# Kernel tuning notes

Hardware: AMD Instinct MI355X
Metric: run time of the kernel (lower is better)

## Reference

```python
import jax, jax.numpy as jnp
import numpy as np

N = 100000   # nodes
E = 1600000  # edges (avg degree 16)
D = 128      # in = hidden = out channels
DROP_P = 0.2


def setup_inputs() -> dict:
    key = jax.random.key(0)
    ks = jax.random.split(key, 11)
    s = 1.0 / np.sqrt(D)  # glorot-ish scale
    inp = {
        "features": jax.random.normal(ks[0], (N, D), jnp.float32),
        "edge_index": jax.random.randint(ks[1], (2, E), 0, N, dtype=jnp.int64),
    }
    for i in range(3):
        inp[f"Wl{i}"] = jax.random.normal(ks[2 + 3 * i], (D, D), jnp.float32) * s
        inp[f"Wr{i}"] = jax.random.normal(ks[3 + 3 * i], (D, D), jnp.float32) * s
        inp[f"b{i}"] = jnp.zeros((D,), jnp.float32)
    return inp


def _sage_conv(x, src, dst, Wl, Wr, b):
    # PyG SAGEConv (aggr='max'): out = lin_l(max_{j->i} x_j) + lin_r(x_i)
    agg = jax.ops.segment_max(x[src], dst, num_segments=N)  # [N, D_in]
    agg = jnp.where(jnp.isfinite(agg), agg, 0.0)  # isolated nodes -> 0 (torch_scatter zero-init)
    return agg @ Wl + x @ Wr + b


def _dropout(x, key, p=DROP_P):
    keep = jax.random.bernoulli(key, 1.0 - p, x.shape)
    return jnp.where(keep, x / (1.0 - p), 0.0)


def reference(features, edge_index, Wl0, Wr0, b0, Wl1, Wr1, b1, Wl2, Wr2, b2):
    src, dst = edge_index[0], edge_index[1]
    k1, k2 = jax.random.split(jax.random.key(42))
    x = _sage_conv(features, src, dst, Wl0, Wr0, b0)
    x = _dropout(jax.nn.elu(x), k1)
    x = _sage_conv(x, src, dst, Wl1, Wr1, b1)
    x = _dropout(jax.nn.elu(x), k2)
    x = _sage_conv(x, src, dst, Wl2, Wr2, b2)
    return x
```

## Files before the change

### kernel.cpp

```cpp
#include <hip/hip_runtime.h>
#include <math.h>

#define D 128
#define BSHIFT 9
#define BCAP 12288

typedef __attribute__((ext_vector_type(8))) _Float16 half8;
typedef __attribute__((ext_vector_type(4))) float floatx4;

__host__ __device__ __forceinline__ unsigned rotl32(unsigned v, int r) {
  return (v << r) | (v >> (32 - r));
}

__host__ __device__ __forceinline__ void threefry2x32(unsigned k0, unsigned k1,
                                                      unsigned x0, unsigned x1,
                                                      unsigned &o0, unsigned &o1) {
  unsigned ks2 = k0 ^ k1 ^ 0x1BD11BDAu;
  unsigned v0 = x0 + k0;
  unsigned v1 = x1 + k1;
  v0 += v1; v1 = rotl32(v1, 13); v1 ^= v0;
  v0 += v1; v1 = rotl32(v1, 15); v1 ^= v0;
  v0 += v1; v1 = rotl32(v1, 26); v1 ^= v0;
  v0 += v1; v1 = rotl32(v1, 6);  v1 ^= v0;
  v0 += k1; v1 += ks2 + 1u;
  v0 += v1; v1 = rotl32(v1, 17); v1 ^= v0;
  v0 += v1; v1 = rotl32(v1, 29); v1 ^= v0;
  v0 += v1; v1 = rotl32(v1, 16); v1 ^= v0;
  v0 += v1; v1 = rotl32(v1, 24); v1 ^= v0;
  v0 += ks2; v1 += k0 + 2u;
  v0 += v1; v1 = rotl32(v1, 13); v1 ^= v0;
  v0 += v1; v1 = rotl32(v1, 15); v1 ^= v0;
  v0 += v1; v1 = rotl32(v1, 26); v1 ^= v0;
  v0 += v1; v1 = rotl32(v1, 6);  v1 ^= v0;
  v0 += k0; v1 += k1 + 3u;
  v0 += v1; v1 = rotl32(v1, 17); v1 ^= v0;
  v0 += v1; v1 = rotl32(v1, 29); v1 ^= v0;
  v0 += v1; v1 = rotl32(v1, 16); v1 ^= v0;
  v0 += v1; v1 = rotl32(v1, 24); v1 ^= v0;
  v0 += k1; v1 += ks2 + 4u;
  v0 += v1; v1 = rotl32(v1, 13); v1 ^= v0;
  v0 += v1; v1 = rotl32(v1, 15); v1 ^= v0;
  v0 += v1; v1 = rotl32(v1, 26); v1 ^= v0;
  v0 += v1; v1 = rotl32(v1, 6);  v1 ^= v0;
  v0 += ks2; v1 += k0 + 5u;
  o0 = v0; o1 = v1;
}

__device__ __forceinline__ unsigned short f2h(float f) {
  _Float16 h = (_Float16)f;
  return *(unsigned short*)&h;
}

__device__ __forceinline__ unsigned pkmax(unsigned a, unsigned b) {
  unsigned r;
  asm("v_pk_max_f16 %0, %1, %2" : "=v"(r) : "v"(a), "v"(b));
  return r;
}


__global__ __launch_bounds__(256) void bucket_count_kernel(
    const int* __restrict__ dst, int* __restrict__ bucketTotal, int nEdges) {
  __shared__ int lc[256];
  int t = threadIdx.x;
  lc[t] = 0;
  __syncthreads();
  int e0 = blockIdx.x * 4096;
  for (int i = t; i < 4096; i += 256) {
    int e = e0 + i;
    if (e < nEdges) atomicAdd(&lc[dst[e] >> BSHIFT], 1);
  }
  __syncthreads();
  int c = lc[t];
  if (c > 0) atomicAdd(&bucketTotal[t], c);
}

__global__ __launch_bounds__(256) void scan_buckets_kernel(
    const int* __restrict__ bucketTotal, int* __restrict__ buckOff,
    int* __restrict__ bucketCursor, int nBuck) {
  __shared__ int s[256];
  int t = threadIdx.x;
  int v = (t < nBuck) ? bucketTotal[t] : 0;
  s[t] = v;
  __syncthreads();
  for (int off = 1; off < 256; off <<= 1) {
    int u = (t >= off) ? s[t - off] : 0;
    __syncthreads();
    s[t] += u;
    __syncthreads();
  }
  int excl = s[t] - v;
  if (t < nBuck) {
    buckOff[t] = excl;
    bucketCursor[t] = excl;
  } else if (t == nBuck) {
    buckOff[t] = s[255];
  }
}

__global__ __launch_bounds__(256) void bucket_scatter_kernel(
    const int* __restrict__ src, const int* __restrict__ dst,
    int* __restrict__ bucketCursor, unsigned* __restrict__ pairs,
    int nEdges, int nBuck) {
  __shared__ int lcount[256];
  __shared__ int lbase[256];
  __shared__ int loff[256];
  int t = threadIdx.x;
  lcount[t] = 0; loff[t] = 0;
  __syncthreads();
  int e0 = blockIdx.x * 4096;
  for (int i = t; i < 4096; i += 256) {
    int e = e0 + i;
    if (e < nEdges) atomicAdd(&lcount[dst[e] >> BSHIFT], 1);
  }
  __syncthreads();
  if (t < nBuck) {
    int c = lcount[t];
    if (c > 0) lbase[t] = atomicAdd(&bucketCursor[t], c);
  }
  __syncthreads();
  for (int i = t; i < 4096; i += 256) {
    int e = e0 + i;
    if (e < nEdges) {
      int d = dst[e];
      int b = d >> BSHIFT;
      int lp = atomicAdd(&loff[b], 1);
      pairs[lbase[b] + lp] = ((unsigned)src[e] << BSHIFT) | ((unsigned)d & 511u);
    }
  }
}

__global__ __launch_bounds__(256) void local_fill_kernel(
    const unsigned* __restrict__ pairs, const int* __restrict__ buckOff,
    int* __restrict__ rowStart, int* __restrict__ csrSrc,
    int nNodes, int nBuck) {
  __shared__ int sData[BCAP];
  __shared__ int lcnt[1 << BSHIFT];
  __shared__ int sSum[256];
  int b = blockIdx.x;
  int node0 = b << BSHIFT;
  int base = buckOff[b];
  int end = buckOff[b + 1];
  int cnt = end - base;
  int t = threadIdx.x;

  lcnt[t] = 0;
  lcnt[t + 256] = 0;
  __syncthreads();

  for (int i = base + t; i < end; i += 256)
    atomicAdd(&lcnt[pairs[i] & 511u], 1);
  __syncthreads();

  int c0 = lcnt[2 * t];
  int c1 = lcnt[2 * t + 1];
  int local = c0 + c1;
  sSum[t] = local;
  __syncthreads();
  for (int off = 1; off < 256; off <<= 1) {
    int v = (t >= off) ? sSum[t - off] : 0;
    __syncthreads();
    sSum[t] += v;
    __syncthreads();
  }
  int excl = sSum[t] - local;
  __syncthreads();
  lcnt[2 * t] = excl;
  lcnt[2 * t + 1] = excl + c0;
  int n0 = node0 + 2 * t;
  int n1 = n0 + 1;
  if (n0 < nNodes) rowStart[n0] = base + excl;
  if (n1 < nNodes) rowStart[n1] = base + excl + c0;
  if (b == nBuck - 1 && t == 255) rowStart[nNodes] = end;
  __syncthreads();

  if (cnt <= BCAP) {
    for (int i = base + t; i < end; i += 256) {
      unsigned p = pairs[i];
      int lp = atomicAdd(&lcnt[p & 511u], 1);
      sData[lp] = (int)(p >> BSHIFT);
    }
    __syncthreads();
    for (int i = t; i < cnt; i += 256)
      csrSrc[base + i] = sData[i];
  } else {
    for (int i = base + t; i < end; i += 256) {
      unsigned p = pairs[i];
      int lp = atomicAdd(&lcnt[p & 511u], 1);
      csrSrc[base + lp] = (int)(p >> BSHIFT);
    }
  }
}

__global__ __launch_bounds__(256) void convert_feat_kernel(
    const float* __restrict__ f, unsigned short* __restrict__ o, int nElems) {
  int i = (blockIdx.x * 256 + threadIdx.x) * 4;
  if (i + 3 < nElems) {
    float4 v = *((const float4*)(f + i));
    unsigned a = (unsigned)f2h(v.x) | ((unsigned)f2h(v.y) << 16);
    unsigned b = (unsigned)f2h(v.z) | ((unsigned)f2h(v.w) << 16);
    *((uint2*)(o + i)) = make_uint2(a, b);
  } else {
    for (int j = i; j < nElems; ++j) o[j] = f2h(f[j]);
  }
}

__global__ __launch_bounds__(256) void pack_weights_kernel(
    const float* __restrict__ Wl0, const float* __restrict__ Wr0,
    const float* __restrict__ Wl1, const float* __restrict__ Wr1,
    const float* __restrict__ Wl2, const float* __restrict__ Wr2,
    unsigned short* __restrict__ Wt) {
  int t = blockIdx.x * 256 + threadIdx.x;
  if (t >= 3 * 128 * 256) return;
  int l = t >> 15;
  int rem = t & 32767;
  int n = rem >> 8;
  int k = rem & 255;
  const float* Wl = (l == 0) ? Wl0 : (l == 1) ? Wl1 : Wl2;
  const float* Wr = (l == 0) ? Wr0 : (l == 1) ? Wr1 : Wr2;
  float v = (k < 128) ? Wl[k * D + n] : Wr[(k - 128) * D + n];
  Wt[t] = f2h(v);
}

__global__ __launch_bounds__(256) void gather_max_f16_kernel(
    const uint4* __restrict__ x8, const int* __restrict__ rowStart,
    const int* __restrict__ csrSrc, uint4* __restrict__ agg8, int nNodes) {
  int n = blockIdx.x * 4 + (threadIdx.x >> 6);
  if (n >= nNodes) return;
  int lane = threadIdx.x & 63;
  int q = lane >> 4;
  int l16 = lane & 15;
  int e0 = rowStart[n], e1 = rowStart[n + 1];
  unsigned m0 = 0xFC00FC00u, m1 = 0xFC00FC00u,
           m2 = 0xFC00FC00u, m3 = 0xFC00FC00u;
  int e = e0;
  for (; e + 7 < e1; e += 8) {
    int sa = csrSrc[e + q];
    int sb = csrSrc[e + 4 + q];
    uint4 va = x8[(size_t)sa * 16 + l16];
    uint4 vb = x8[(size_t)sb * 16 + l16];
    m0 = pkmax(m0, pkmax(va.x, vb.x));
    m1 = pkmax(m1, pkmax(va.y, vb.y));
    m2 = pkmax(m2, pkmax(va.z, vb.z));
    m3 = pkmax(m3, pkmax(va.w, vb.w));
  }
  if (e + 3 < e1) {
    int sa = csrSrc[e + q];
    uint4 va = x8[(size_t)sa * 16 + l16];
    m0 = pkmax(m0, va.x); m1 = pkmax(m1, va.y);
    m2 = pkmax(m2, va.z); m3 = pkmax(m3, va.w);
    e += 4;
  }
  for (; e < e1; ++e) {
    int sa = csrSrc[e];
    uint4 va = x8[(size_t)sa * 16 + l16];
    m0 = pkmax(m0, va.x); m1 = pkmax(m1, va.y);
    m2 = pkmax(m2, va.z); m3 = pkmax(m3, va.w);
  }
  m0 = pkmax(m0, (unsigned)__shfl_xor((int)m0, 16, 64));
  m1 = pkmax(m1, (unsigned)__shfl_xor((int)m1, 16, 64));
  m2 = pkmax(m2, (unsigned)__shfl_xor((int)m2, 16, 64));
  m3 = pkmax(m3, (unsigned)__shfl_xor((int)m3, 16, 64));
  m0 = pkmax(m0, (unsigned)__shfl_xor((int)m0, 32, 64));
  m1 = pkmax(m1, (unsigned)__shfl_xor((int)m1, 32, 64));
  m2 = pkmax(m2, (unsigned)__shfl_xor((int)m2, 32, 64));
  m3 = pkmax(m3, (unsigned)__shfl_xor((int)m3, 32, 64));
  uint4 r = make_uint4(0u, 0u, 0u, 0u);
  if (e0 != e1) r = make_uint4(m0, m1, m2, m3);
  if (q == 0) agg8[(size_t)n * 16 + l16] = r;
}

#define PA 280

__global__ __launch_bounds__(256) void fused_mfma_kernel(
    const unsigned short* __restrict__ agghf, unsigned short* __restrict__ xhf,
    const unsigned short* __restrict__ Wt, const float* __restrict__ bias,
    float* __restrict__ outF, int nRows, int mode, unsigned kk0, unsigned kk1) {
  __shared__ unsigned short sA[32 * PA];

  const int tid = threadIdx.x;
  const int row0 = blockIdx.x * 32;
  const int wv = tid >> 6, lane = tid & 63;
  const int quad = lane >> 4, m16 = lane & 15;
  const int nbase = wv * 32;

#pragma unroll
  for (int i = 0; i < 4; ++i) {
    int idx = i * 256 + tid;
    int r = idx >> 5;
    int seg = idx & 31;
    uint4 v = make_uint4(0, 0, 0, 0);
    if (row0 + r < nRows) {
      if (seg < 16) v = ((const uint4*)(agghf + (size_t)(row0 + r) * D))[seg];
      else          v = ((const uint4*)(xhf  + (size_t)(row0 + r) * D))[seg - 16];
    }
    *((uint4*)(sA + r * PA + seg * 8)) = v;
  }

  half8 bfr[2][4][2];
#pragma unroll
  for (int kc = 0; kc < 2; ++kc)
#pragma unroll
    for (int ks = 0; ks < 4; ++ks)
#pragma unroll
      for (int j = 0; j < 2; ++j)
        bfr[kc][ks][j] = *((const half8*)(
            Wt + (size_t)(nbase + j * 16 + m16) * 256 + kc * 128 + ks * 32 + quad * 8));

  floatx4 acc[2][2];
#pragma unroll
  for (int i = 0; i < 2; ++i)
#pragma unroll
    for (int j = 0; j < 2; ++j) acc[i][j] = (floatx4)(0.0f);

  __syncthreads();

#pragma unroll
  for (int kc = 0; kc < 2; ++kc)
#pragma unroll
    for (int ks = 0; ks < 4; ++ks) {
      int kA = kc * 128 + ks * 32 + quad * 8;
      half8 a0 = *((const half8*)(sA + m16 * PA + kA));
      half8 a1 = *((const half8*)(sA + (m16 + 16) * PA + kA));
      acc[0][0] = __builtin_amdgcn_mfma_f32_16x16x32_f16(a0, bfr[kc][ks][0], acc[0][0], 0, 0, 0);
      acc[0][1] = __builtin_amdgcn_mfma_f32_16x16x32_f16(a0, bfr[kc][ks][1], acc[0][1], 0, 0, 0);
      acc[1][0] = __builtin_amdgcn_mfma_f32_16x16x32_f16(a1, bfr[kc][ks][0], acc[1][0], 0, 0, 0);
      acc[1][1] = __builtin_amdgcn_mfma_f32_16x16x32_f16(a1, bfr[kc][ks][1], acc[1][1], 0, 0, 0);
    }

#pragma unroll
  for (int j = 0; j < 2; ++j) {
    int col = nbase + j * 16 + m16;
    float bc = bias[col];
#pragma unroll
    for (int i = 0; i < 2; ++i) {
#pragma unroll
      for (int reg = 0; reg < 4; ++reg) {
        int r = row0 + i * 16 + quad * 4 + reg;
        if (r >= nRows) continue;
        float v = acc[i][j][reg] + bc;
        if (mode < 2) {
          v = (v > 0.0f) ? v : expm1f(v);
          unsigned jj = (unsigned)r * D + col;
          unsigned y0, y1;
          threefry2x32(kk0, kk1, 0u, jj, y0, y1);
          float u = __uint_as_float((((y0 ^ y1) >> 9)) | 0x3F800000u) - 1.0f;
          v = (u < 0.8f) ? v * 1.25f : 0.0f;
          xhf[(size_t)r * D + col] = f2h(v);
        } else {
          outF[(size_t)r * D + col] = v;
        }
      }
    }
  }
}

extern "C" void kernel_launch(void* const* d_in, const int* in_sizes, int n_in,
                              void* d_out, int out_size, void* d_ws, size_t ws_size,
                              hipStream_t stream) {
  const float* feat = (const float*)d_in[0];
  const int* ei = (const int*)d_in[1];
  const float* Wl0 = (const float*)d_in[2];
  const float* Wr0 = (const float*)d_in[3];
  const float* b0 = (const float*)d_in[4];
  const float* Wl1 = (const float*)d_in[5];
  const float* Wr1 = (const float*)d_in[6];
  const float* b1 = (const float*)d_in[7];
  const float* Wl2 = (const float*)d_in[8];
  const float* Wr2 = (const float*)d_in[9];
  const float* b2 = (const float*)d_in[10];

  const int N = in_sizes[0] / D;
  const int E = in_sizes[1] / 2;
  const int* src = ei;
  const int* dst = ei + E;

  const size_t hfBytes = (size_t)N * D * 2;
  char* wsp = (char*)d_ws;
  size_t off = 0;
  unsigned short* xhf   = (unsigned short*)(wsp + off); off += hfBytes;
  unsigned short* agghf = (unsigned short*)(wsp + off); off += hfBytes;
  unsigned short* Wt    = (unsigned short*)(wsp + off); off += ((size_t)3 * 128 * 256 * 2 + 511) & ~511ull;
  int* rowStart     = (int*)(wsp + off); off += ((size_t)(N + 1) * 4 + 511) & ~511ull;
  int* bucketTotal  = (int*)(wsp + off); off += 2048;
  int* buckOff      = (int*)(wsp + off); off += 2048;
  int* bucketCursor = (int*)(wsp + off); off += 2048;
  int* csrSrc    = (int*)(wsp + off); off += (size_t)E * 4;
  unsigned* pairs = (unsigned*)(wsp + off); off += (size_t)E * 4;

  const int nBuck = (N + (1 << BSHIFT) - 1) >> BSHIFT;

  unsigned k1a, k1b, k2a, k2b;
  threefry2x32(0u, 42u, 0u, 0u, k1a, k1b);
  threefry2x32(0u, 42u, 0u, 1u, k2a, k2b);

  hipMemsetAsync(bucketTotal, 0, 1024, stream);
  bucket_count_kernel<<<(E + 4095) / 4096, 256, 0, stream>>>(dst, bucketTotal, E);
  scan_buckets_kernel<<<1, 256, 0, stream>>>(bucketTotal, buckOff, bucketCursor, nBuck);
  bucket_scatter_kernel<<<(E + 4095) / 4096, 256, 0, stream>>>(src, dst, bucketCursor, pairs, E, nBuck);
  local_fill_kernel<<<nBuck, 256, 0, stream>>>(pairs, buckOff, rowStart, csrSrc, N, nBuck);

  convert_feat_kernel<<<(N * D / 4 + 255) / 256, 256, 0, stream>>>(feat, xhf, N * D);
  pack_weights_kernel<<<(3 * 128 * 256 + 255) / 256, 256, 0, stream>>>(
      Wl0, Wr0, Wl1, Wr1, Wl2, Wr2, Wt);

  dim3 blk(256);
  dim3 grdMax((N + 3) / 4);
  dim3 grdGemm((N + 31) / 32);
  float* outF = (float*)d_out;

  gather_max_f16_kernel<<<grdMax, blk, 0, stream>>>((const uint4*)xhf, rowStart, csrSrc, (uint4*)agghf, N);
  fused_mfma_kernel<<<grdGemm, blk, 0, stream>>>(agghf, xhf, Wt, b0, outF, N, 0, k1a, k1b);

  gather_max_f16_kernel<<<grdMax, blk, 0, stream>>>((const uint4*)xhf, rowStart, csrSrc, (uint4*)agghf, N);
  fused_mfma_kernel<<<grdGemm, blk, 0, stream>>>(agghf, xhf, Wt + 32768, b1, outF, N, 1, k2a, k2b);

  gather_max_f16_kernel<<<grdMax, blk, 0, stream>>>((const uint4*)xhf, rowStart, csrSrc, (uint4*)agghf, N);
  fused_mfma_kernel<<<grdGemm, blk, 0, stream>>>(agghf, xhf, Wt + 65536, b2, outF, N, 2, 0u, 0u);
}
```

Measured before the change: 521.9 us.

## Fuse neighbor max-gather into the MFMA layer kernel with ping-pong buffers

Merges the separate gather-max kernel into the GEMM kernel: each block gathers max-aggregated neighbor rows for its 32 nodes straight into shared memory, then runs the MFMA and epilogue. Two feature buffers are ping-ponged so a layer never overwrites inputs other blocks still read. This removes the agg buffer write and read round trip and three launches per run. The gather now runs with 8 rows per wave serially inside a larger block, which may cut memory-level parallelism and latency hiding. The change also swaps expm1f for __expf-1, which is cheaper but slightly less accurate near zero.

```diff
diff --git a/kernel.cpp b/kernel.cpp
--- a/kernel.cpp
+++ b/kernel.cpp
@@ -221,58 +221,11 @@
   Wt[t] = f2h(v);
 }
 
-__global__ __launch_bounds__(256) void gather_max_f16_kernel(
-    const uint4* __restrict__ x8, const int* __restrict__ rowStart,
-    const int* __restrict__ csrSrc, uint4* __restrict__ agg8, int nNodes) {
-  int n = blockIdx.x * 4 + (threadIdx.x >> 6);
-  if (n >= nNodes) return;
-  int lane = threadIdx.x & 63;
-  int q = lane >> 4;
-  int l16 = lane & 15;
-  int e0 = rowStart[n], e1 = rowStart[n + 1];
-  unsigned m0 = 0xFC00FC00u, m1 = 0xFC00FC00u,
-           m2 = 0xFC00FC00u, m3 = 0xFC00FC00u;
-  int e = e0;
-  for (; e + 7 < e1; e += 8) {
-    int sa = csrSrc[e + q];
-    int sb = csrSrc[e + 4 + q];
-    uint4 va = x8[(size_t)sa * 16 + l16];
-    uint4 vb = x8[(size_t)sb * 16 + l16];
-    m0 = pkmax(m0, pkmax(va.x, vb.x));
-    m1 = pkmax(m1, pkmax(va.y, vb.y));
-    m2 = pkmax(m2, pkmax(va.z, vb.z));
-    m3 = pkmax(m3, pkmax(va.w, vb.w));
-  }
-  if (e + 3 < e1) {
-    int sa = csrSrc[e + q];
-    uint4 va = x8[(size_t)sa * 16 + l16];
-    m0 = pkmax(m0, va.x); m1 = pkmax(m1, va.y);
-    m2 = pkmax(m2, va.z); m3 = pkmax(m3, va.w);
-    e += 4;
-  }
-  for (; e < e1; ++e) {
-    int sa = csrSrc[e];
-    uint4 va = x8[(size_t)sa * 16 + l16];
-    m0 = pkmax(m0, va.x); m1 = pkmax(m1, va.y);
-    m2 = pkmax(m2, va.z); m3 = pkmax(m3, va.w);
-  }
-  m0 = pkmax(m0, (unsigned)__shfl_xor((int)m0, 16, 64));
-  m1 = pkmax(m1, (unsigned)__shfl_xor((int)m1, 16, 64));
-  m2 = pkmax(m2, (unsigned)__shfl_xor((int)m2, 16, 64));
-  m3 = pkmax(m3, (unsigned)__shfl_xor((int)m3, 16, 64));
-  m0 = pkmax(m0, (unsigned)__shfl_xor((int)m0, 32, 64));
-  m1 = pkmax(m1, (unsigned)__shfl_xor((int)m1, 32, 64));
-  m2 = pkmax(m2, (unsigned)__shfl_xor((int)m2, 32, 64));
-  m3 = pkmax(m3, (unsigned)__shfl_xor((int)m3, 32, 64));
-  uint4 r = make_uint4(0u, 0u, 0u, 0u);
-  if (e0 != e1) r = make_uint4(m0, m1, m2, m3);
-  if (q == 0) agg8[(size_t)n * 16 + l16] = r;
-}
-
 #define PA 280
 
-__global__ __launch_bounds__(256) void fused_mfma_kernel(
-    const unsigned short* __restrict__ agghf, unsigned short* __restrict__ xhf,
+__global__ __launch_bounds__(256) void fused_layer_kernel(
+    const unsigned short* __restrict__ xin, unsigned short* __restrict__ yout,
+    const int* __restrict__ rowStart, const int* __restrict__ csrSrc,
     const unsigned short* __restrict__ Wt, const float* __restrict__ bias,
     float* __restrict__ outF, int nRows, int mode, unsigned kk0, unsigned kk1) {
   __shared__ unsigned short sA[32 * PA];
@@ -282,18 +235,62 @@
   const int wv = tid >> 6, lane = tid & 63;
   const int quad = lane >> 4, m16 = lane & 15;
   const int nbase = wv * 32;
-
-#pragma unroll
-  for (int i = 0; i < 4; ++i) {
+  const uint4* x4 = (const uint4*)xin;
+
+#pragma unroll
+  for (int i = 0; i < 2; ++i) {
     int idx = i * 256 + tid;
-    int r = idx >> 5;
-    int seg = idx & 31;
+    int r = idx >> 4;
+    int seg = idx & 15;
     uint4 v = make_uint4(0, 0, 0, 0);
-    if (row0 + r < nRows) {
-      if (seg < 16) v = ((const uint4*)(agghf + (size_t)(row0 + r) * D))[seg];
-      else          v = ((const uint4*)(xhf  + (size_t)(row0 + r) * D))[seg - 16];
-    }
-    *((uint4*)(sA + r * PA + seg * 8)) = v;
+    if (row0 + r < nRows) v = x4[(size_t)(row0 + r) * 16 + seg];
+    *((uint4*)(sA + r * PA + 128 + seg * 8)) = v;
+  }
+
+  const int q = quad;
+  const int l16 = m16;
+  for (int rr = 0; rr < 8; ++rr) {
+    int r = (wv << 3) + rr;
+    int n = row0 + r;
+    int e0 = 0, e1 = 0;
+    if (n < nRows) { e0 = rowStart[n]; e1 = rowStart[n + 1]; }
+    unsigned m0 = 0xFC00FC00u, m1 = 0xFC00FC00u,
+             m2 = 0xFC00FC00u, m3 = 0xFC00FC00u;
+    int e = e0;
+    for (; e + 7 < e1; e += 8) {
+      int sa = csrSrc[e + q];
+      int sb = csrSrc[e + 4 + q];
+      uint4 va = x4[(size_t)sa * 16 + l16];
+      uint4 vb = x4[(size_t)sb * 16 + l16];
+      m0 = pkmax(m0, pkmax(va.x, vb.x));
+      m1 = pkmax(m1, pkmax(va.y, vb.y));
+      m2 = pkmax(m2, pkmax(va.z, vb.z));
+      m3 = pkmax(m3, pkmax(va.w, vb.w));
+    }
+    if (e + 3 < e1) {
+      int sa = csrSrc[e + q];
+      uint4 va = x4[(size_t)sa * 16 + l16];
+      m0 = pkmax(m0, va.x); m1 = pkmax(m1, va.y);
+      m2 = pkmax(m2, va.z); m3 = pkmax(m3, va.w);
+      e += 4;
+    }
+    for (; e < e1; ++e) {
+      int sa = csrSrc[e];
+      uint4 va = x4[(size_t)sa * 16 + l16];
+      m0 = pkmax(m0, va.x); m1 = pkmax(m1, va.y);
+      m2 = pkmax(m2, va.z); m3 = pkmax(m3, va.w);
+    }
+    m0 = pkmax(m0, (unsigned)__shfl_xor((int)m0, 16, 64));
+    m1 = pkmax(m1, (unsigned)__shfl_xor((int)m1, 16, 64));
+    m2 = pkmax(m2, (unsigned)__shfl_xor((int)m2, 16, 64));
+    m3 = pkmax(m3, (unsigned)__shfl_xor((int)m3, 16, 64));
+    m0 = pkmax(m0, (unsigned)__shfl_xor((int)m0, 32, 64));
+    m1 = pkmax(m1, (unsigned)__shfl_xor((int)m1, 32, 64));
+    m2 = pkmax(m2, (unsigned)__shfl_xor((int)m2, 32, 64));
+    m3 = pkmax(m3, (unsigned)__shfl_xor((int)m3, 32, 64));
+    uint4 res = make_uint4(0u, 0u, 0u, 0u);
+    if (e0 != e1) res = make_uint4(m0, m1, m2, m3);
+    if (q == 0) *((uint4*)(sA + r * PA + l16 * 8)) = res;
   }
 
   half8 bfr[2][4][2];
@@ -339,13 +336,13 @@
         if (r >= nRows) continue;
         float v = acc[i][j][reg] + bc;
         if (mode < 2) {
-          v = (v > 0.0f) ? v : expm1f(v);
+          v = (v > 0.0f) ? v : (__expf(v) - 1.0f);
           unsigned jj = (unsigned)r * D + col;
           unsigned y0, y1;
           threefry2x32(kk0, kk1, 0u, jj, y0, y1);
           float u = __uint_as_float((((y0 ^ y1) >> 9)) | 0x3F800000u) - 1.0f;
           v = (u < 0.8f) ? v * 1.25f : 0.0f;
-          xhf[(size_t)r * D + col] = f2h(v);
+          yout[(size_t)r * D + col] = f2h(v);
         } else {
           outF[(size_t)r * D + col] = v;
         }
@@ -377,9 +374,9 @@
   const size_t hfBytes = (size_t)N * D * 2;
   char* wsp = (char*)d_ws;
   size_t off = 0;
-  unsigned short* xhf   = (unsigned short*)(wsp + off); off += hfBytes;
-  unsigned short* agghf = (unsigned short*)(wsp + off); off += hfBytes;
-  unsigned short* Wt    = (unsigned short*)(wsp + off); off += ((size_t)3 * 128 * 256 * 2 + 511) & ~511ull;
+  unsigned short* x0 = (unsigned short*)(wsp + off); off += hfBytes;
+  unsigned short* x1 = (unsigned short*)(wsp + off); off += hfBytes;
+  unsigned short* Wt = (unsigned short*)(wsp + off); off += ((size_t)3 * 128 * 256 * 2 + 511) & ~511ull;
   int* rowStart     = (int*)(wsp + off); off += ((size_t)(N + 1) * 4 + 511) & ~511ull;
   int* bucketTotal  = (int*)(wsp + off); off += 2048;
   int* buckOff      = (int*)(wsp + off); off += 2048;
@@ -399,21 +396,18 @@
   bucket_scatter_kernel<<<(E + 4095) / 4096, 256, 0, stream>>>(src, dst, bucketCursor, pairs, E, nBuck);
   local_fill_kernel<<<nBuck, 256, 0, stream>>>(pairs, buckOff, rowStart, csrSrc, N, nBuck);
 
-  convert_feat_kernel<<<(N * D / 4 + 255) / 256, 256, 0, stream>>>(feat, xhf, N * D);
+  convert_feat_kernel<<<(N * D / 4 + 255) / 256, 256, 0, stream>>>(feat, x0, N * D);
   pack_weights_kernel<<<(3 * 128 * 256 + 255) / 256, 256, 0, stream>>>(
       Wl0, Wr0, Wl1, Wr1, Wl2, Wr2, Wt);
 
   dim3 blk(256);
-  dim3 grdMax((N + 3) / 4);
   dim3 grdGemm((N + 31) / 32);
   float* outF = (float*)d_out;
 
-  gather_max_f16_kernel<<<grdMax, blk, 0, stream>>>((const uint4*)xhf, rowStart, csrSrc, (uint4*)agghf, N);
-  fused_mfma_kernel<<<grdGemm, blk, 0, stream>>>(agghf, xhf, Wt, b0, outF, N, 0, k1a, k1b);
-
-  gather_max_f16_kernel<<<grdMax, blk, 0, stream>>>((const uint4*)xhf, rowStart, csrSrc, (uint4*)agghf, N);
-  fused_mfma_kernel<<<grdGemm, blk, 0, stream>>>(agghf, xhf, Wt + 32768, b1, outF, N, 1, k2a, k2b);
-
-  gather_max_f16_kernel<<<grdMax, blk, 0, stream>>>((const uint4*)xhf, rowStart, csrSrc, (uint4*)agghf, N);
-  fused_mfma_kernel<<<grdGemm, blk, 0, stream>>>(agghf, xhf, Wt + 65536, b2, outF, N, 2, 0u, 0u);
-}
+  fused_layer_kernel<<<grdGemm, blk, 0, stream>>>(
+      x0, x1, rowStart, csrSrc, Wt, b0, outF, N, 0, k1a, k1b);
+  fused_layer_kernel<<<grdGemm, blk, 0, stream>>>(
+      x1, x0, rowStart, csrSrc, Wt + 32768, b1, outF, N, 1, k2a, k2b);
+  fused_layer_kernel<<<grdGemm, blk, 0, stream>>>(
+      x0, x1, rowStart, csrSrc, Wt + 65536, b2, outF, N, 2, 0u, 0u);
+}
```

Result: slower. 610.8 us (+17.0%).

## Enlarge GEMM row tile and stage fp16 output through shared memory

Applied to the files above, without the earlier changes.

The fused MFMA kernel now processes 64 rows per block instead of 32, so each B-fragment weight load from global memory is reused across twice as many rows. For the ELU+dropout modes, results are written into the shared A tile and then stored to global memory as coalesced 16-byte vectors, replacing scattered 2-byte stores. expm1f is replaced with __expf(v)-1, which is cheaper but less accurate near zero. The larger tile doubles shared memory and accumulator registers per block, and launch_bounds now requests 2 blocks per SM.

```diff
diff --git a/kernel.cpp b/kernel.cpp
--- a/kernel.cpp
+++ b/kernel.cpp
@@ -270,21 +270,22 @@
 }
 
 #define PA 280
-
-__global__ __launch_bounds__(256) void fused_mfma_kernel(
+#define TROWS 64
+
+__global__ __launch_bounds__(256, 2) void fused_mfma_kernel(
     const unsigned short* __restrict__ agghf, unsigned short* __restrict__ xhf,
     const unsigned short* __restrict__ Wt, const float* __restrict__ bias,
     float* __restrict__ outF, int nRows, int mode, unsigned kk0, unsigned kk1) {
-  __shared__ unsigned short sA[32 * PA];
+  __shared__ unsigned short sA[TROWS * PA];
 
   const int tid = threadIdx.x;
-  const int row0 = blockIdx.x * 32;
+  const int row0 = blockIdx.x * TROWS;
   const int wv = tid >> 6, lane = tid & 63;
   const int quad = lane >> 4, m16 = lane & 15;
   const int nbase = wv * 32;
 
 #pragma unroll
-  for (int i = 0; i < 4; ++i) {
+  for (int i = 0; i < 8; ++i) {
     int idx = i * 256 + tid;
     int r = idx >> 5;
     int seg = idx & 31;
@@ -306,9 +307,9 @@
         bfr[kc][ks][j] = *((const half8*)(
             Wt + (size_t)(nbase + j * 16 + m16) * 256 + kc * 128 + ks * 32 + quad * 8));
 
-  floatx4 acc[2][2];
-#pragma unroll
-  for (int i = 0; i < 2; ++i)
+  floatx4 acc[4][2];
+#pragma unroll
+  for (int i = 0; i < 4; ++i)
 #pragma unroll
     for (int j = 0; j < 2; ++j) acc[i][j] = (floatx4)(0.0f);
 
@@ -319,35 +320,59 @@
 #pragma unroll
     for (int ks = 0; ks < 4; ++ks) {
       int kA = kc * 128 + ks * 32 + quad * 8;
-      half8 a0 = *((const half8*)(sA + m16 * PA + kA));
-      half8 a1 = *((const half8*)(sA + (m16 + 16) * PA + kA));
-      acc[0][0] = __builtin_amdgcn_mfma_f32_16x16x32_f16(a0, bfr[kc][ks][0], acc[0][0], 0, 0, 0);
-      acc[0][1] = __builtin_amdgcn_mfma_f32_16x16x32_f16(a0, bfr[kc][ks][1], acc[0][1], 0, 0, 0);
-      acc[1][0] = __builtin_amdgcn_mfma_f32_16x16x32_f16(a1, bfr[kc][ks][0], acc[1][0], 0, 0, 0);
-      acc[1][1] = __builtin_amdgcn_mfma_f32_16x16x32_f16(a1, bfr[kc][ks][1], acc[1][1], 0, 0, 0);
-    }
-
-#pragma unroll
-  for (int j = 0; j < 2; ++j) {
-    int col = nbase + j * 16 + m16;
-    float bc = bias[col];
-#pragma unroll
-    for (int i = 0; i < 2; ++i) {
-#pragma unroll
-      for (int reg = 0; reg < 4; ++reg) {
-        int r = row0 + i * 16 + quad * 4 + reg;
-        if (r >= nRows) continue;
-        float v = acc[i][j][reg] + bc;
-        if (mode < 2) {
-          v = (v > 0.0f) ? v : expm1f(v);
-          unsigned jj = (unsigned)r * D + col;
+#pragma unroll
+      for (int i = 0; i < 4; ++i) {
+        half8 a = *((const half8*)(sA + (m16 + 16 * i) * PA + kA));
+        acc[i][0] = __builtin_amdgcn_mfma_f32_16x16x32_f16(a, bfr[kc][ks][0], acc[i][0], 0, 0, 0);
+        acc[i][1] = __builtin_amdgcn_mfma_f32_16x16x32_f16(a, bfr[kc][ks][1], acc[i][1], 0, 0, 0);
+      }
+    }
+
+  if (mode < 2) {
+    __syncthreads();
+#pragma unroll
+    for (int j = 0; j < 2; ++j) {
+      int col = nbase + j * 16 + m16;
+      float bc = bias[col];
+#pragma unroll
+      for (int i = 0; i < 4; ++i) {
+#pragma unroll
+        for (int reg = 0; reg < 4; ++reg) {
+          int r = i * 16 + quad * 4 + reg;
+          if (row0 + r >= nRows) continue;
+          float v = acc[i][j][reg] + bc;
+          v = (v > 0.0f) ? v : (__expf(v) - 1.0f);
+          unsigned jj = (unsigned)(row0 + r) * D + col;
           unsigned y0, y1;
           threefry2x32(kk0, kk1, 0u, jj, y0, y1);
           float u = __uint_as_float((((y0 ^ y1) >> 9)) | 0x3F800000u) - 1.0f;
           v = (u < 0.8f) ? v * 1.25f : 0.0f;
-          xhf[(size_t)r * D + col] = f2h(v);
-        } else {
-          outF[(size_t)r * D + col] = v;
+          sA[r * PA + col] = f2h(v);
+        }
+      }
+    }
+    __syncthreads();
+#pragma unroll
+    for (int i = 0; i < 4; ++i) {
+      int idx = i * 256 + tid;
+      int r = idx >> 4;
+      int seg = idx & 15;
+      if (row0 + r < nRows)
+        ((uint4*)xhf)[(size_t)(row0 + r) * 16 + seg] =
+            *((const uint4*)(sA + r * PA + seg * 8));
+    }
+  } else {
+#pragma unroll
+    for (int j = 0; j < 2; ++j) {
+      int col = nbase + j * 16 + m16;
+      float bc = bias[col];
+#pragma unroll
+      for (int i = 0; i < 4; ++i) {
+#pragma unroll
+        for (int reg = 0; reg < 4; ++reg) {
+          int r = row0 + i * 16 + quad * 4 + reg;
+          if (r >= nRows) continue;
+          outF[(size_t)r * D + col] = acc[i][j][reg] + bc;
         }
       }
     }
@@ -405,7 +430,7 @@
 
   dim3 blk(256);
   dim3 grdMax((N + 3) / 4);
-  dim3 grdGemm((N + 31) / 32);
+  dim3 grdGemm((N + TROWS - 1) / TROWS);
   float* outF = (float*)d_out;
 
   gather_max_f16_kernel<<<grdMax, blk, 0, stream>>>((const uint4*)xhf, rowStart, csrSrc, (uint4*)agghf, N);
```

Measured after the change: 497.3 us. 1.05x faster.
